# Performance work log

Hardware: AMD Instinct MI355X
Metric: run time of the kernel (lower is better)

The kernel has to match this reference:

```python
import jax, jax.numpy as jnp
import numpy as np

B, L, D = 32768, 256, 16  # batch, chain length, bond dim; physical dim d=2


def setup_inputs() -> dict:
    key = jax.random.key(0)
    k_phi, k_first, k_mid, k_last = jax.random.split(key, 4)
    scale = 1.0 / np.sqrt(2.0 * D)  # variance-preserving chain
    phi_batch = jax.random.normal(k_phi, (B, L, 2), dtype=jnp.float32)
    core_first = jax.random.normal(k_first, (2, D), dtype=jnp.float32) * scale
    cores_mid = jax.random.normal(k_mid, (L - 2, D, 2, D), dtype=jnp.float32) * scale
    core_last = jax.random.normal(k_last, (D, 2), dtype=jnp.float32) * scale
    out_bias = jnp.zeros((), dtype=jnp.float32)
    return {
        "phi_batch": phi_batch,
        "core_first": core_first,
        "cores_mid": cores_mid,
        "core_last": core_last,
        "out_bias": out_bias,
    }


def reference(phi_batch, core_first, cores_mid, core_last, out_bias):
    # MPS / tensor-train contraction, batched over samples.
    # Each sample contracts feature vectors phi[i] (len-2) into the physical
    # index of core i, then chains the resulting D x D matrices via a
    # left-to-right bond-space matvec (what cotengra would find per-sample).
    # v0: [B, D] = phi[:,0] contracted with first core [2, D]
    v0 = jnp.einsum("bp,pd->bd", phi_batch[:, 0], core_first)

    # middle features, scan-major layout: [L-2, B, 2]
    phis_mid = jnp.swapaxes(phi_batch[:, 1:-1], 0, 1)

    def step(v, xs):
        phi_t, core = xs  # phi_t: [B, 2], core: [D, 2, D]
        # contract bond then physical index; never materialize [B, D, D]
        u = jnp.einsum("bq,qpr->bpr", v, core)   # [B, 2, D]
        v_new = jnp.einsum("bp,bpr->br", phi_t, u)  # [B, D]
        return v_new, None

    v, _ = jax.lax.scan(step, v0, (phis_mid, cores_mid))

    # close the chain with last core [D, 2] and last feature [B, 2]
    out = jnp.einsum("bq,qp,bp->b", v, core_last, phi_batch[:, -1])
    return out + out_bias
```

## Files before the change

### kernel.cpp

```cpp
#include <hip/hip_runtime.h>
#include <stdint.h>


typedef short  bf16x8 __attribute__((ext_vector_type(8)));
typedef float  f32x4  __attribute__((ext_vector_type(4)));
typedef int    i32x4  __attribute__((ext_vector_type(4)));
typedef unsigned int u32;

#define NPF 64
#define NPB 63
#define BWD_OFF (NPF*4*64)

#define PACK_HI(hi, lo) ((int)__builtin_amdgcn_perm((u32)(hi), (u32)(lo), 0x07060302u))

__device__ __forceinline__ u32 rne_bump(u32 u){ return u + 0x7FFFu + ((u >> 16) & 1u); }

__global__ void build_pair_frags(const float* __restrict__ cm, i32x4* __restrict__ ws)
{
  __shared__ float Ca[512], Cb[512];
  const int bid = blockIdx.x;
  const bool fwd = bid < NPF;
  const int j  = fwd ? bid : bid - NPF;
  const int ta = fwd ? 2*j     : 252 - 2*j;
  const int tb = fwd ? 2*j + 1 : 253 - 2*j;
  {
    const float* A = cm + ta*512;
    const float* B = cm + tb*512;
    for (int i = threadIdx.x; i < 512; i += 256){ Ca[i] = A[i]; Cb[i] = B[i]; }
  }
  __syncthreads();
  const int f    = threadIdx.x >> 6;
  const int lane = threadIdx.x & 63;
  const int m    = lane & 15;
  const int g    = lane >> 4;
  const int p    = f >> 1, q = f & 1;
  u32 hi[4], lo[4];
  #pragma unroll
  for (int x = 0; x < 4; ++x){
    const int cq = 4*g + x;
    float acc = 0.f;
    #pragma unroll
    for (int r = 0; r < 16; ++r){
      const float a = fwd ? Ca[cq*32 + p*16 + r] : Ca[m*32 + p*16 + r];
      const float b = fwd ? Cb[r*32 + q*16 + m]  : Cb[r*32 + q*16 + cq];
      acc = fmaf(a, b, acc);
    }
    const u32 u  = __float_as_uint(acc);
    const u32 aa = rne_bump(u);
    const float hf = __uint_as_float(aa & 0xFFFF0000u);
    const u32 bb = rne_bump(__float_as_uint(acc - hf));
    hi[x] = aa >> 16; lo[x] = bb >> 16;
  }
  i32x4 w;
  w[0] = (int)(hi[0] | (hi[1] << 16));
  w[1] = (int)(hi[2] | (hi[3] << 16));
  w[2] = (int)(lo[0] | (lo[1] << 16));
  w[3] = (int)(lo[2] | (lo[3] << 16));
  ws[(fwd ? 0 : BWD_OFF) + (j*4 + f)*64 + lane] = w;
}

__device__ __forceinline__ void make_bfrag(const float (&v)[4], i32x4 &bfr)
{
  const u32 u0 = __float_as_uint(v[0]), u1 = __float_as_uint(v[1]);
  const u32 u2 = __float_as_uint(v[2]), u3 = __float_as_uint(v[3]);
  const float l0 = v[0] - __uint_as_float(u0 & 0xFFFF0000u);
  const float l1 = v[1] - __uint_as_float(u1 & 0xFFFF0000u);
  const float l2 = v[2] - __uint_as_float(u2 & 0xFFFF0000u);
  const float l3 = v[3] - __uint_as_float(u3 & 0xFFFF0000u);
  bfr[0] = PACK_HI(u1, u0);
  bfr[1] = PACK_HI(u3, u2);
  bfr[2] = PACK_HI(__float_as_uint(l1), __float_as_uint(l0));
  bfr[3] = PACK_HI(__float_as_uint(l3), __float_as_uint(l2));
}

__device__ __forceinline__ void pair_step(
    const i32x4 &G0, const i32x4 &G1, const i32x4 &G2, const i32x4 &G3,
    float2 cA, float2 cB, float (&v)[4], i32x4 &bfr)
{
  const float c00 = cA.x*cB.x, c01 = cA.x*cB.y;
  const float c10 = cA.y*cB.x, c11 = cA.y*cB.y;
  i32x4 sw; sw[0]=bfr[2]; sw[1]=bfr[3]; sw[2]=bfr[0]; sw[3]=bfr[1];
  const bf16x8 bh = __builtin_bit_cast(bf16x8, bfr);
  const bf16x8 bs = __builtin_bit_cast(bf16x8, sw);
  const f32x4 z = {0.f,0.f,0.f,0.f};
  f32x4 a00 = __builtin_amdgcn_mfma_f32_16x16x32_bf16(__builtin_bit_cast(bf16x8,G0), bh, z, 0,0,0);
  a00 = __builtin_amdgcn_mfma_f32_16x16x32_bf16(__builtin_bit_cast(bf16x8,G0), bs, a00, 0,0,0);
  f32x4 a01 = __builtin_amdgcn_mfma_f32_16x16x32_bf16(__builtin_bit_cast(bf16x8,G1), bh, z, 0,0,0);
  a01 = __builtin_amdgcn_mfma_f32_16x16x32_bf16(__builtin_bit_cast(bf16x8,G1), bs, a01, 0,0,0);
  f32x4 a10 = __builtin_amdgcn_mfma_f32_16x16x32_bf16(__builtin_bit_cast(bf16x8,G2), bh, z, 0,0,0);
  a10 = __builtin_amdgcn_mfma_f32_16x16x32_bf16(__builtin_bit_cast(bf16x8,G2), bs, a10, 0,0,0);
  f32x4 a11 = __builtin_amdgcn_mfma_f32_16x16x32_bf16(__builtin_bit_cast(bf16x8,G3), bh, z, 0,0,0);
  a11 = __builtin_amdgcn_mfma_f32_16x16x32_bf16(__builtin_bit_cast(bf16x8,G3), bs, a11, 0,0,0);
  #pragma unroll
  for (int i2 = 0; i2 < 4; ++i2)
    v[i2] = c00*a00[i2] + c01*a01[i2] + c10*a10[i2] + c11*a11[i2];
  make_bfrag(v, bfr);
}

__global__ __launch_bounds__(256, 2) void mps_chain(
  const float* __restrict__ phi,
  const float* __restrict__ core_first,
  const float* __restrict__ core_last,
  const float* __restrict__ bias,
  const i32x4* __restrict__ ws,
  float* __restrict__ out)
{
  const int lane = threadIdx.x & 63;
  const int wv   = threadIdx.x >> 6;
  const int n    = lane & 15;
  const int g    = lane >> 4;
  const bool isFwd = (wv < 2);
  const int dirIdx = isFwd ? 0 : 1;
  const int sb   = blockIdx.x * 64 + (wv & 1) * 32;

  __shared__ float red[128*20];

  const i32x4* wsD    = isFwd ? ws : (ws + BWD_OFF);
  const int    maxPr  = isFwd ? NPF - 1 : NPB - 1;
  const i32x4* wsLane = wsD + lane;

  const float* phiSrc0 = phi + (size_t)(sb + n) * 512 + g * 4;

  const int qtF  = isFwd ? 0 : 1;
  const int aQ   = ((lane & 15) + 16*qtF) << 2;
  const int adrA0 = isFwd ? aQ       : aQ + 64;
  const int adrB0 = isFwd ? aQ + 64  : aQ + 128;
  const int adrA1 = isFwd ? aQ + 64  : aQ;
  const int adrB1 = isFwd ? aQ + 128 : aQ + 64;

  float vch[2][4];
  i32x4 bfr[2];

  #pragma unroll
  for (int k = 0; k < 2; ++k){
    const float* pr = phi + (size_t)(sb + 16*k + n) * 512;
    if (isFwd){
      const float2 p0 = *(const float2*)pr;
      #pragma unroll
      for (int reg = 0; reg < 4; ++reg){
        const int r = g*4 + reg;
        vch[k][reg] = p0.x * core_first[r] + p0.y * core_first[16 + r];
      }
    } else {
      const float2 pL = *(const float2*)(pr + 510);
      #pragma unroll
      for (int reg = 0; reg < 4; ++reg){
        const int r = g*4 + reg;
        vch[k][reg] = pL.x * core_last[2*r] + pL.y * core_last[2*r + 1];
      }
    }
    make_bfrag(vch[k], bfr[k]);
  }

  i32x4 GA0, GA1, GA2, GA3;
  i32x4 GB0, GB1, GB2, GB3;
  f32x4 phiC[2], phiN[2];

  { const i32x4* s = wsLane;        GA0=s[0]; GA1=s[64]; GA2=s[128]; GA3=s[192]; }
  { const i32x4* s = wsLane + 256;  GB0=s[0]; GB1=s[64]; GB2=s[128]; GB3=s[192]; }
  #pragma unroll
  for (int k = 0; k < 2; ++k){
    const float* ps = phiSrc0 + (size_t)k * 16 * 512;
    phiC[k] = *(const f32x4*)(ps + (isFwd ? 0 : 496));
    phiN[k] = *(const f32x4*)(ps + (isFwd ? 8 : 488));
  }
  __builtin_amdgcn_sched_barrier(0);

  #pragma unroll 1
  for (int c = 0; c < 32; ++c){
    float2 cA0[2], cB0[2], cA1[2], cB1[2];
    #pragma unroll
    for (int k = 0; k < 2; ++k){
      #define SPULL(e, adr) __int_as_float(__builtin_amdgcn_ds_bpermute((adr), __float_as_int(phiC[k][e])))
      cA0[k] = make_float2(SPULL(2, adrA0), SPULL(3, adrA0));
      cB0[k] = make_float2(SPULL(0, adrB0), SPULL(1, adrB0));
      cA1[k] = make_float2(SPULL(2, adrA1), SPULL(3, adrA1));
      cB1[k] = make_float2(SPULL(0, adrB1), SPULL(1, adrB1));
      #undef SPULL
    }

    #pragma unroll
    for (int k = 0; k < 2; ++k)
      pair_step(GA0, GA1, GA2, GA3, cA0[k], cB0[k], vch[k], bfr[k]);
    { const int j = 2*c + 2;
      const i32x4* s = wsLane + (j > maxPr ? maxPr : j) * 256;
      GA0=s[0]; GA1=s[64]; GA2=s[128]; GA3=s[192]; }
    __builtin_amdgcn_sched_barrier(0);

    if (isFwd || (2*c + 1) < NPB){
      #pragma unroll
      for (int k = 0; k < 2; ++k)
        pair_step(GB0, GB1, GB2, GB3, cA1[k], cB1[k], vch[k], bfr[k]);
    }
    { const int j = 2*c + 3;
      const i32x4* s = wsLane + (j > maxPr ? maxPr : j) * 256;
      GB0=s[0]; GB1=s[64]; GB2=s[128]; GB3=s[192]; }

    #pragma unroll
    for (int k = 0; k < 2; ++k) phiC[k] = phiN[k];
    { const int cc = (c + 2 > 31) ? 31 : (c + 2);
      #pragma unroll
      for (int k = 0; k < 2; ++k){
        const float* ps = phiSrc0 + (size_t)k * 16 * 512;
        phiN[k] = *(const f32x4*)(ps + (isFwd ? 8*cc : 496 - 8*cc));
      } }
    __builtin_amdgcn_sched_barrier(0);
  }

  #pragma unroll
  for (int k = 0; k < 2; ++k)
    *(float4*)&red[(dirIdx*64 + (wv & 1)*32 + 16*k + n)*20 + 4*g] =
        make_float4(vch[k][0], vch[k][1], vch[k][2], vch[k][3]);
  __syncthreads();
  if (threadIdx.x < 64){
    const int s = threadIdx.x;
    float acc = bias[0];
    #pragma unroll
    for (int qq = 0; qq < 16; ++qq)
      acc += red[s*20 + qq] * red[(64 + s)*20 + qq];
    out[blockIdx.x*64 + s] = acc;
  }
}

extern "C" void kernel_launch(void* const* d_in, const int* in_sizes, int n_in,
                              void* d_out, int out_size, void* d_ws, size_t ws_size,
                              hipStream_t stream)
{
  const float* phi  = (const float*)d_in[0];
  const float* cf   = (const float*)d_in[1];
  const float* cm   = (const float*)d_in[2];
  const float* cl   = (const float*)d_in[3];
  const float* bias = (const float*)d_in[4];
  i32x4* ws = (i32x4*)d_ws;

  build_pair_frags<<<NPF + NPB, 256, 0, stream>>>(cm, ws);
  mps_chain<<<512, 256, 0, stream>>>(phi, cf, cl, bias, ws, (float*)d_out);
}
```

Before: 137.4 us.

## Interleave two sample chains' MFMAs and load phi coefficients directly per lane

Merges the per-chain pair_step into pair_step2, which interleaves the MFMA sequences of the two independent 16-sample chains so their dependency latencies overlap. It replaces the ds_bpermute shuffles of phi values with direct float2 global loads per lane, and it restructures the loop into 31 iterations plus a peeled tail, dropping the sched_barriers and the per-iteration branch. The cost it targets is MFMA latency stalls and LDS permute traffic. In exchange there are more redundant global loads of phi, higher register pressure from the prefetched next-step fragments, and scheduling left to the compiler.

```diff
diff --git a/kernel.cpp b/kernel.cpp
--- a/kernel.cpp
+++ b/kernel.cpp
@@ -73,28 +73,35 @@
   bfr[3] = PACK_HI(__float_as_uint(l3), __float_as_uint(l2));
 }
 
-__device__ __forceinline__ void pair_step(
+#define MFMA_(G,Bv,Cv) __builtin_amdgcn_mfma_f32_16x16x32_bf16(__builtin_bit_cast(bf16x8,(G)), (Bv), (Cv), 0,0,0)
+
+__device__ __forceinline__ void pair_step2(
     const i32x4 &G0, const i32x4 &G1, const i32x4 &G2, const i32x4 &G3,
-    float2 cA, float2 cB, float (&v)[4], i32x4 &bfr)
-{
-  const float c00 = cA.x*cB.x, c01 = cA.x*cB.y;
-  const float c10 = cA.y*cB.x, c11 = cA.y*cB.y;
-  i32x4 sw; sw[0]=bfr[2]; sw[1]=bfr[3]; sw[2]=bfr[0]; sw[3]=bfr[1];
-  const bf16x8 bh = __builtin_bit_cast(bf16x8, bfr);
-  const bf16x8 bs = __builtin_bit_cast(bf16x8, sw);
+    float2 cAa, float2 cBa, float2 cAb, float2 cBb,
+    float (&vA)[4], float (&vB)[4], i32x4 &bA, i32x4 &bB)
+{
+  i32x4 sA; sA[0]=bA[2]; sA[1]=bA[3]; sA[2]=bA[0]; sA[3]=bA[1];
+  i32x4 sB; sB[0]=bB[2]; sB[1]=bB[3]; sB[2]=bB[0]; sB[3]=bB[1];
+  const bf16x8 hA = __builtin_bit_cast(bf16x8,bA), wA = __builtin_bit_cast(bf16x8,sA);
+  const bf16x8 hB = __builtin_bit_cast(bf16x8,bB), wB = __builtin_bit_cast(bf16x8,sB);
   const f32x4 z = {0.f,0.f,0.f,0.f};
-  f32x4 a00 = __builtin_amdgcn_mfma_f32_16x16x32_bf16(__builtin_bit_cast(bf16x8,G0), bh, z, 0,0,0);
-  a00 = __builtin_amdgcn_mfma_f32_16x16x32_bf16(__builtin_bit_cast(bf16x8,G0), bs, a00, 0,0,0);
-  f32x4 a01 = __builtin_amdgcn_mfma_f32_16x16x32_bf16(__builtin_bit_cast(bf16x8,G1), bh, z, 0,0,0);
-  a01 = __builtin_amdgcn_mfma_f32_16x16x32_bf16(__builtin_bit_cast(bf16x8,G1), bs, a01, 0,0,0);
-  f32x4 a10 = __builtin_amdgcn_mfma_f32_16x16x32_bf16(__builtin_bit_cast(bf16x8,G2), bh, z, 0,0,0);
-  a10 = __builtin_amdgcn_mfma_f32_16x16x32_bf16(__builtin_bit_cast(bf16x8,G2), bs, a10, 0,0,0);
-  f32x4 a11 = __builtin_amdgcn_mfma_f32_16x16x32_bf16(__builtin_bit_cast(bf16x8,G3), bh, z, 0,0,0);
-  a11 = __builtin_amdgcn_mfma_f32_16x16x32_bf16(__builtin_bit_cast(bf16x8,G3), bs, a11, 0,0,0);
+  f32x4 a0A = MFMA_(G0,hA,z);   f32x4 a0B = MFMA_(G0,hB,z);
+  a0A = MFMA_(G0,wA,a0A);       a0B = MFMA_(G0,wB,a0B);
+  f32x4 a1A = MFMA_(G1,hA,z);   f32x4 a1B = MFMA_(G1,hB,z);
+  a1A = MFMA_(G1,wA,a1A);       a1B = MFMA_(G1,wB,a1B);
+  f32x4 a2A = MFMA_(G2,hA,z);   f32x4 a2B = MFMA_(G2,hB,z);
+  a2A = MFMA_(G2,wA,a2A);       a2B = MFMA_(G2,wB,a2B);
+  f32x4 a3A = MFMA_(G3,hA,z);   f32x4 a3B = MFMA_(G3,hB,z);
+  a3A = MFMA_(G3,wA,a3A);       a3B = MFMA_(G3,wB,a3B);
+  const float c00A=cAa.x*cBa.x, c01A=cAa.x*cBa.y, c10A=cAa.y*cBa.x, c11A=cAa.y*cBa.y;
+  const float c00B=cAb.x*cBb.x, c01B=cAb.x*cBb.y, c10B=cAb.y*cBb.x, c11B=cAb.y*cBb.y;
   #pragma unroll
-  for (int i2 = 0; i2 < 4; ++i2)
-    v[i2] = c00*a00[i2] + c01*a01[i2] + c10*a10[i2] + c11*a11[i2];
-  make_bfrag(v, bfr);
+  for (int i = 0; i < 4; ++i){
+    vA[i] = c00A*a0A[i] + c01A*a1A[i] + c10A*a2A[i] + c11A*a3A[i];
+    vB[i] = c00B*a0B[i] + c01B*a1B[i] + c10B*a2B[i] + c11B*a3B[i];
+  }
+  make_bfrag(vA, bA);
+  make_bfrag(vB, bB);
 }
 
 __global__ __launch_bounds__(256, 2) void mps_chain(
@@ -119,98 +126,80 @@
   const int    maxPr  = isFwd ? NPF - 1 : NPB - 1;
   const i32x4* wsLane = wsD + lane;
 
-  const float* phiSrc0 = phi + (size_t)(sb + n) * 512 + g * 4;
-
-  const int qtF  = isFwd ? 0 : 1;
-  const int aQ   = ((lane & 15) + 16*qtF) << 2;
-  const int adrA0 = isFwd ? aQ       : aQ + 64;
-  const int adrB0 = isFwd ? aQ + 64  : aQ + 128;
-  const int adrA1 = isFwd ? aQ + 64  : aQ;
-  const int adrB1 = isFwd ? aQ + 128 : aQ + 64;
-
-  float vch[2][4];
-  i32x4 bfr[2];
-
-  #pragma unroll
-  for (int k = 0; k < 2; ++k){
-    const float* pr = phi + (size_t)(sb + 16*k + n) * 512;
+  const float*  row0 = phi + (size_t)(sb + n) * 512;
+  const float*  row1 = phi + (size_t)(sb + 16 + n) * 512;
+  const float2* c20  = (const float2*)row0;
+  const float2* c21  = (const float2*)row1;
+
+  const int uB = isFwd ? 1 : 253;
+  const int vB = isFwd ? 3 : 251;
+  const int st = isFwd ? 4 : -4;
+
+  float vA[4], vBv[4];
+  i32x4 bA, bB;
+  {
     if (isFwd){
-      const float2 p0 = *(const float2*)pr;
+      const float2 p0 = *(const float2*)row0;
+      const float2 p1 = *(const float2*)row1;
       #pragma unroll
-      for (int reg = 0; reg < 4; ++reg){
-        const int r = g*4 + reg;
-        vch[k][reg] = p0.x * core_first[r] + p0.y * core_first[16 + r];
+      for (int r = 0; r < 4; ++r){
+        const int rr = g*4 + r;
+        vA[r]  = p0.x * core_first[rr] + p0.y * core_first[16 + rr];
+        vBv[r] = p1.x * core_first[rr] + p1.y * core_first[16 + rr];
       }
     } else {
-      const float2 pL = *(const float2*)(pr + 510);
+      const float2 p0 = *(const float2*)(row0 + 510);
+      const float2 p1 = *(const float2*)(row1 + 510);
       #pragma unroll
-      for (int reg = 0; reg < 4; ++reg){
-        const int r = g*4 + reg;
-        vch[k][reg] = pL.x * core_last[2*r] + pL.y * core_last[2*r + 1];
+      for (int r = 0; r < 4; ++r){
+        const int rr = g*4 + r;
+        vA[r]  = p0.x * core_last[2*rr] + p0.y * core_last[2*rr + 1];
+        vBv[r] = p1.x * core_last[2*rr] + p1.y * core_last[2*rr + 1];
       }
     }
-    make_bfrag(vch[k], bfr[k]);
-  }
-
-  i32x4 GA0, GA1, GA2, GA3;
-  i32x4 GB0, GB1, GB2, GB3;
-  f32x4 phiC[2], phiN[2];
-
-  { const i32x4* s = wsLane;        GA0=s[0]; GA1=s[64]; GA2=s[128]; GA3=s[192]; }
-  { const i32x4* s = wsLane + 256;  GB0=s[0]; GB1=s[64]; GB2=s[128]; GB3=s[192]; }
-  #pragma unroll
-  for (int k = 0; k < 2; ++k){
-    const float* ps = phiSrc0 + (size_t)k * 16 * 512;
-    phiC[k] = *(const f32x4*)(ps + (isFwd ? 0 : 496));
-    phiN[k] = *(const f32x4*)(ps + (isFwd ? 8 : 488));
-  }
-  __builtin_amdgcn_sched_barrier(0);
+    make_bfrag(vA, bA);
+    make_bfrag(vBv, bB);
+  }
+
+  i32x4 A0,A1,A2,A3, B0,B1,B2,B3;
+  float2 eA0, eB0, eA1, eB1;
+  float2 oA0, oB0, oA1, oB1;
+
+  { const i32x4* s = wsLane;        A0=s[0]; A1=s[64]; A2=s[128]; A3=s[192]; }
+  { const i32x4* s = wsLane + 256;  B0=s[0]; B1=s[64]; B2=s[128]; B3=s[192]; }
+  eA0 = c20[uB];     eB0 = c20[uB + 1];
+  eA1 = c21[uB];     eB1 = c21[uB + 1];
+  oA0 = c20[vB];     oB0 = c20[vB + 1];
+  oA1 = c21[vB];     oB1 = c21[vB + 1];
 
   #pragma unroll 1
-  for (int c = 0; c < 32; ++c){
-    float2 cA0[2], cB0[2], cA1[2], cB1[2];
-    #pragma unroll
-    for (int k = 0; k < 2; ++k){
-      #define SPULL(e, adr) __int_as_float(__builtin_amdgcn_ds_bpermute((adr), __float_as_int(phiC[k][e])))
-      cA0[k] = make_float2(SPULL(2, adrA0), SPULL(3, adrA0));
-      cB0[k] = make_float2(SPULL(0, adrB0), SPULL(1, adrB0));
-      cA1[k] = make_float2(SPULL(2, adrA1), SPULL(3, adrA1));
-      cB1[k] = make_float2(SPULL(0, adrB1), SPULL(1, adrB1));
-      #undef SPULL
-    }
-
-    #pragma unroll
-    for (int k = 0; k < 2; ++k)
-      pair_step(GA0, GA1, GA2, GA3, cA0[k], cB0[k], vch[k], bfr[k]);
-    { const int j = 2*c + 2;
-      const i32x4* s = wsLane + (j > maxPr ? maxPr : j) * 256;
-      GA0=s[0]; GA1=s[64]; GA2=s[128]; GA3=s[192]; }
-    __builtin_amdgcn_sched_barrier(0);
-
-    if (isFwd || (2*c + 1) < NPB){
-      #pragma unroll
-      for (int k = 0; k < 2; ++k)
-        pair_step(GB0, GB1, GB2, GB3, cA1[k], cB1[k], vch[k], bfr[k]);
-    }
-    { const int j = 2*c + 3;
-      const i32x4* s = wsLane + (j > maxPr ? maxPr : j) * 256;
-      GB0=s[0]; GB1=s[64]; GB2=s[128]; GB3=s[192]; }
-
-    #pragma unroll
-    for (int k = 0; k < 2; ++k) phiC[k] = phiN[k];
-    { const int cc = (c + 2 > 31) ? 31 : (c + 2);
-      #pragma unroll
-      for (int k = 0; k < 2; ++k){
-        const float* ps = phiSrc0 + (size_t)k * 16 * 512;
-        phiN[k] = *(const f32x4*)(ps + (isFwd ? 8*cc : 496 - 8*cc));
-      } }
-    __builtin_amdgcn_sched_barrier(0);
-  }
-
-  #pragma unroll
-  for (int k = 0; k < 2; ++k)
-    *(float4*)&red[(dirIdx*64 + (wv & 1)*32 + 16*k + n)*20 + 4*g] =
-        make_float4(vch[k][0], vch[k][1], vch[k][2], vch[k][3]);
+  for (int c = 0; c < 31; ++c){
+    i32x4 nA0,nA1,nA2,nA3, nB0,nB1,nB2,nB3;
+    { const i32x4* s = wsLane + (2*c + 2) * 256;
+      nA0=s[0]; nA1=s[64]; nA2=s[128]; nA3=s[192]; }
+    { int j3 = 2*c + 3; if (j3 > maxPr) j3 = maxPr;
+      const i32x4* s = wsLane + j3 * 256;
+      nB0=s[0]; nB1=s[64]; nB2=s[128]; nB3=s[192]; }
+    const int u1 = uB + st*(c+1), v1 = vB + st*(c+1);
+    const float2 neA0 = c20[u1], neB0 = c20[u1+1], neA1 = c21[u1], neB1 = c21[u1+1];
+    const float2 noA0 = c20[v1], noB0 = c20[v1+1], noA1 = c21[v1], noB1 = c21[v1+1];
+
+    pair_step2(A0,A1,A2,A3, eA0,eB0, eA1,eB1, vA,vBv, bA,bB);
+    pair_step2(B0,B1,B2,B3, oA0,oB0, oA1,oB1, vA,vBv, bA,bB);
+
+    A0=nA0; A1=nA1; A2=nA2; A3=nA3;  B0=nB0; B1=nB1; B2=nB2; B3=nB3;
+    eA0=neA0; eB0=neB0; eA1=neA1; eB1=neB1;
+    oA0=noA0; oB0=noB0; oA1=noA1; oB1=noB1;
+  }
+
+  pair_step2(A0,A1,A2,A3, eA0,eB0, eA1,eB1, vA,vBv, bA,bB);
+  if (isFwd)
+    pair_step2(B0,B1,B2,B3, oA0,oB0, oA1,oB1, vA,vBv, bA,bB);
+
+  *(float4*)&red[(dirIdx*64 + (wv & 1)*32 + n)*20 + 4*g] =
+      make_float4(vA[0], vA[1], vA[2], vA[3]);
+  *(float4*)&red[(dirIdx*64 + (wv & 1)*32 + 16 + n)*20 + 4*g] =
+      make_float4(vBv[0], vBv[1], vBv[2], vBv[3]);
   __syncthreads();
   if (threadIdx.x < 64){
     const int s = threadIdx.x;
```

Measured after the change: 166.6 us. +21.3%, slower.
